# Kernel optimization log

Hardware: AMD Instinct MI355X
Metric: run time of the kernel (lower is better)

Reference implementation:

```python
import jax, jax.numpy as jnp
import numpy as np

AMP = 2  # from init_kwargs

def setup_inputs() -> dict:
    key = jax.random.key(0)
    k1, k2 = jax.random.split(key)
    B, C, H, W = 4, 32, 256, 256
    x_q = jax.random.normal(k1, (B, C, H, W), dtype=jnp.float32)
    x_k = jax.random.normal(k2, (B, C, H, W), dtype=jnp.float32)
    return {"x_q": x_q, "x_k": x_k, "num_heads": 4}


def reference(x_q, x_k, num_heads):
    amp = AMP
    ks = 2 * amp + 1  # kernel_size
    B, C, H, W = x_q.shape
    head_dim = C // num_heads
    scale = head_dim ** (-0.5)
    # (B, head_dim, heads, H, W)
    q = x_q.reshape(B, head_dim, num_heads, H, W) * scale
    k = x_k.reshape(B, head_dim, num_heads, H, W)
    k_pad = jnp.pad(k, ((0, 0), (0, 0), (0, 0), (amp, amp), (amp, amp)))
    # validity mask: padded region is invalid (mask < 0.5 in original)
    valid = jnp.pad(jnp.ones((H, W), dtype=x_q.dtype), ((amp, amp), (amp, amp)))
    attn = []
    for i in range(ks):  # static loop over 25 offsets
        for j in range(ks):
            # per-offset dot product over head_dim -> (B, heads, H, W)
            a = jnp.sum(q * k_pad[:, :, :, i:i + H, j:j + W], axis=1)
            a = jnp.where(valid[i:i + H, j:j + W] > 0.5, a, jnp.asarray(-1000.0, a.dtype))
            attn.append(a)
    attn = jnp.stack(attn, axis=1)          # (B, ks*ks, heads, H, W)
    attn = jax.nn.softmax(attn, axis=1)
    # offset grid: arange(-s//2+1, s//2+1) == [-amp, ..., amp]
    offs = jnp.arange(-amp, amp + 1, dtype=x_q.dtype)
    grid = jnp.stack(jnp.meshgrid(offs, offs, indexing='ij'), axis=-1).reshape(ks * ks, 2)
    # offset-weighted sum over the ks*ks window positions -> (B, 2, heads, H, W)
    v_ = jnp.einsum('bkhxy,kc->bchxy', attn, grid)
    # mean over heads -> (B, 2, H, W)
    return jnp.mean(v_, axis=2)
```

## Files before the change

### kernel.cpp

```cpp
#include <hip/hip_runtime.h>

#define Bdim 4
#define Cdim 32
#define NH   4
#define HD   8
#define Hdim 256
#define Wdim 256
#define AMP  2
#define KS   5

#define XT    32
#define TY    8
#define TROWS 12
#define TPOS  44
#define NPAIRS 16
#define PAIR_STRIDE (TROWS * TPOS)
#define TILE_SLOTS (NPAIRS * PAIR_STRIDE)

typedef _Float16 h2 __attribute__((ext_vector_type(2)));

static __device__ __forceinline__ float dot2acc(h2 a, h2 b, float c) {
#if __has_builtin(__builtin_amdgcn_fdot2)
    return __builtin_amdgcn_fdot2(a, b, c, false);
#else
    return c + (float)a.x * (float)b.x + (float)a.y * (float)b.y;
#endif
}

__global__ __launch_bounds__(256) void natt_offset_kernel(
    const float* __restrict__ xq,
    const float* __restrict__ xk,
    float* __restrict__ out)
{
    __shared__ __align__(16) float kt[TILE_SLOTS];

    const int tid = threadIdx.x;
    const int bid = blockIdx.x;
    const int r8  = bid & 7;
    const int u   = bid >> 3;
    const int yt  = r8 * 4 + (u & 3);
    const int rst = u >> 2;
    const int xt  = rst & 7;
    const int b   = rst >> 3;

    const int Y0 = yt * TY;
    const int X0 = xt * XT;
    const bool interior = (yt != 0) && (yt != 31) && (xt != 0) && (xt != 7);

    const int h    = tid >> 6;
    const int lane = tid & 63;
    const int row  = lane >> 3;
    const int qx   = lane & 7;
    const int y    = Y0 + row;
    const int x0   = X0 + qx * 4;

    const size_t plane = (size_t)Hdim * Wdim;
    const float scale = 0.35355339059327373f;

    {
        const float* kb = xk + (size_t)b * Cdim * plane;
        if (interior) {
            #pragma unroll
            for (int it = 0; it < 8; ++it) {
                const int j = lane + it * 64;
                if (j < NPAIRS / 4 * TROWS * 10) {
                    const int c4 = j % 10;
                    const int t  = j / 10;
                    const int rw = t % TROWS;
                    const int d2 = t / TROWS;
                    const int c0 = 8 * d2 + h;
                    const int yr = Y0 - AMP + rw;
                    const int xs = X0 - 6 + c4 * 4;
                    const float* pa = kb + (size_t)c0 * plane + (size_t)yr * Wdim + xs;
                    const float4 va = *(const float4*)pa;
                    const float4 vb = *(const float4*)(pa + 4 * plane);
                    const float a[4]  = {va.x, va.y, va.z, va.w};
                    const float bb[4] = {vb.x, vb.y, vb.z, vb.w};
                    float o[4];
                    #pragma unroll
                    for (int k2 = 0; k2 < 4; ++k2) {
                        h2 pk;
                        pk.x = (_Float16)a[k2];
                        pk.y = (_Float16)bb[k2];
                        o[k2] = __builtin_bit_cast(float, pk);
                    }
                    *(float4*)(kt + ((d2 << 2) | h) * PAIR_STRIDE + rw * TPOS + c4 * 4) =
                        make_float4(o[0], o[1], o[2], o[3]);
                }
            }
        } else {
            #pragma unroll
            for (int it = 0; it < 8; ++it) {
                const int j = lane + it * 64;
                if (j < NPAIRS / 4 * TROWS * 10) {
                    const int c4 = j % 10;
                    const int t  = j / 10;
                    const int rw = t % TROWS;
                    const int d2 = t / TROWS;
                    const int c0 = 8 * d2 + h;
                    int yr = Y0 - AMP + rw;
                    yr = yr < 0 ? 0 : (yr > Hdim - 1 ? Hdim - 1 : yr);
                    const int xs = X0 - 6 + c4 * 4;
                    const int xc = xs < 0 ? 0 : (xs > Wdim - 4 ? Wdim - 4 : xs);
                    const int sh = xs - xc;
                    const float* pa = kb + (size_t)c0 * plane + (size_t)yr * Wdim + xc;
                    const float4 va = *(const float4*)pa;
                    const float4 vb = *(const float4*)(pa + 4 * plane);
                    const float a[4]  = {va.x, va.y, va.z, va.w};
                    const float bb[4] = {vb.x, vb.y, vb.z, vb.w};
                    float o[4];
                    #pragma unroll
                    for (int k2 = 0; k2 < 4; ++k2) {
                        int idx = k2 + sh;
                        idx = idx < 0 ? 0 : (idx > 3 ? 3 : idx);
                        h2 pk;
                        pk.x = (_Float16)a[idx];
                        pk.y = (_Float16)bb[idx];
                        o[k2] = __builtin_bit_cast(float, pk);
                    }
                    *(float4*)(kt + ((d2 << 2) | h) * PAIR_STRIDE + rw * TPOS + c4 * 4) =
                        make_float4(o[0], o[1], o[2], o[3]);
                }
            }
        }
    }

    const float* qb = xq + (size_t)b * Cdim * plane + (size_t)y * Wdim + x0;
    h2 q2[4][4];
    #pragma unroll
    for (int d2 = 0; d2 < 4; ++d2) {
        const float4 qa = *(const float4*)(qb + (size_t)((2 * d2)     * NH + h) * plane);
        const float4 qc = *(const float4*)(qb + (size_t)((2 * d2 + 1) * NH + h) * plane);
        const float qa4[4] = {qa.x, qa.y, qa.z, qa.w};
        const float qc4[4] = {qc.x, qc.y, qc.z, qc.w};
        #pragma unroll
        for (int p = 0; p < 4; ++p) {
            q2[d2][p].x = (_Float16)(qa4[p] * scale);
            q2[d2][p].y = (_Float16)(qc4[p] * scale);
        }
    }


    float Z[4]  = {0.f, 0.f, 0.f, 0.f};
    float sx[4] = {0.f, 0.f, 0.f, 0.f};
    float sy[4] = {0.f, 0.f, 0.f, 0.f};

    #pragma unroll
    for (int r = 0; r < KS; ++r) {
        float dot[KS][4];
        #pragma unroll
        for (int dj = 0; dj < KS; ++dj) {
            dot[dj][0] = 0.f; dot[dj][1] = 0.f; dot[dj][2] = 0.f; dot[dj][3] = 0.f;
        }

        #pragma unroll
        for (int d2 = 0; d2 < 4; ++d2) {
            const float* wp = kt + ((d2 << 2) | h) * PAIR_STRIDE
                                 + (row + r) * TPOS + (qx * 4 + 4);
            const float4 wa = *(const float4*)wp;
            const float4 wb = *(const float4*)(wp + 4);
            const float wf[8] = {wa.x, wa.y, wa.z, wa.w, wb.x, wb.y, wb.z, wb.w};
            h2 w[8];
            #pragma unroll
            for (int k2 = 0; k2 < 8; ++k2) w[k2] = __builtin_bit_cast(h2, wf[k2]);
            #pragma unroll
            for (int dj = 0; dj < KS; ++dj) {
                #pragma unroll
                for (int p = 0; p < 4; ++p)
                    dot[dj][p] = dot2acc(q2[d2][p], w[p + dj], dot[dj][p]);
            }
        }

        const float fdi = (float)(r - AMP);
        if (interior) {
            #pragma unroll
            for (int p = 0; p < 4; ++p) {
                float e[KS];
                #pragma unroll
                for (int dj = 0; dj < KS; ++dj) e[dj] = __expf(dot[dj][p]);
                const float er = ((e[0] + e[1]) + (e[2] + e[3])) + e[4];
                Z[p]  += er;
                sx[p] += fdi * er;
                sy[p] += (e[3] - e[1]) + 2.f * (e[4] - e[0]);
            }
        } else {
            const int yy = y + r - AMP;
            const bool rowok = (yy >= 0) && (yy < Hdim);
            #pragma unroll
            for (int p = 0; p < 4; ++p) {
                float e[KS];
                #pragma unroll
                for (int dj = 0; dj < KS; ++dj) {
                    const int xx = x0 + p + dj - AMP;
                    const bool ok = rowok && (xx >= 0) && (xx < Wdim);
                    e[dj] = ok ? __expf(dot[dj][p]) : 0.f;
                }
                const float er = ((e[0] + e[1]) + (e[2] + e[3])) + e[4];
                Z[p]  += er;
                sx[p] += fdi * er;
                sy[p] += (e[3] - e[1]) + 2.f * (e[4] - e[0]);
            }
        }
    }

    __syncthreads();
    float* red = kt;
    const int pxl = row * XT + qx * 4;
    {
        const float i0 = 1.f / Z[0], i1 = 1.f / Z[1], i2 = 1.f / Z[2], i3 = 1.f / Z[3];
        *(float4*)(red + (h * 2 + 0) * (XT * TY) + pxl) =
            make_float4(sx[0]*i0, sx[1]*i1, sx[2]*i2, sx[3]*i3);
        *(float4*)(red + (h * 2 + 1) * (XT * TY) + pxl) =
            make_float4(sy[0]*i0, sy[1]*i1, sy[2]*i2, sy[3]*i3);
    }
    __syncthreads();

    if (h < 2) {
        float acc[4] = {0.f, 0.f, 0.f, 0.f};
        #pragma unroll
        for (int hh = 0; hh < NH; ++hh) {
            const float4 v = *(const float4*)(red + (hh * 2 + h) * (XT * TY) + pxl);
            acc[0] += v.x; acc[1] += v.y; acc[2] += v.z; acc[3] += v.w;
        }
        *(float4*)(out + ((size_t)b * 2 + h) * plane + (size_t)y * Wdim + x0) =
            make_float4(acc[0]*0.25f, acc[1]*0.25f, acc[2]*0.25f, acc[3]*0.25f);
    }
}

extern "C" void kernel_launch(void* const* d_in, const int* in_sizes, int n_in,
                              void* d_out, int out_size, void* d_ws, size_t ws_size,
                              hipStream_t stream) {
    const float* xq = (const float*)d_in[0];
    const float* xk = (const float*)d_in[1];
    float* out = (float*)d_out;

    natt_offset_kernel<<<dim3(1024, 1, 1), dim3(256, 1, 1), 0, stream>>>(xq, xk, out);
}
```

Before: 101.8 us.

## Split heads into separate 64-thread blocks and reduce heads with atomics

Each 256-thread block covering four heads becomes four 64-thread blocks, one per head, each holding a smaller shared K tile with tighter padding. The shared-memory cross-head reduction and its two barriers are replaced by float atomicAdds into an output that a new kernel zeroes first. The aim is more blocks, lower LDS per block and no block-level sync. In exchange it adds a second launch, four-way atomic contention per output element, and a summation order that is no longer deterministic.

```diff
diff --git a/kernel.cpp b/kernel.cpp
--- a/kernel.cpp
+++ b/kernel.cpp
@@ -12,8 +12,8 @@
 #define XT    32
 #define TY    8
 #define TROWS 12
-#define TPOS  44
-#define NPAIRS 16
+#define TPOS  40
+#define NPAIRS 4
 #define PAIR_STRIDE (TROWS * TPOS)
 #define TILE_SLOTS (NPAIRS * PAIR_STRIDE)
 
@@ -27,32 +27,36 @@
 #endif
 }
 
-__global__ __launch_bounds__(256) void natt_offset_kernel(
+__global__ __launch_bounds__(256) void zero_out_kernel(float* __restrict__ out) {
+    ((float4*)out)[blockIdx.x * 256 + threadIdx.x] = make_float4(0.f, 0.f, 0.f, 0.f);
+}
+
+__global__ __launch_bounds__(64, 4) void natt_head_kernel(
     const float* __restrict__ xq,
     const float* __restrict__ xk,
     float* __restrict__ out)
 {
     __shared__ __align__(16) float kt[TILE_SLOTS];
 
-    const int tid = threadIdx.x;
-    const int bid = blockIdx.x;
-    const int r8  = bid & 7;
+    const int lane = threadIdx.x;
+    const int bid  = blockIdx.x;
+    const int xcd = bid & 7;
     const int u   = bid >> 3;
-    const int yt  = r8 * 4 + (u & 3);
-    const int rst = u >> 2;
-    const int xt  = rst & 7;
-    const int b   = rst >> 3;
+    const int yt  = xcd * 4 + (u & 3);
+    const int v   = u >> 2;
+    const int xt  = v & 7;
+    const int w2  = v >> 3;
+    const int h   = w2 & 3;
+    const int b   = w2 >> 2;
 
     const int Y0 = yt * TY;
     const int X0 = xt * XT;
     const bool interior = (yt != 0) && (yt != 31) && (xt != 0) && (xt != 7);
 
-    const int h    = tid >> 6;
-    const int lane = tid & 63;
-    const int row  = lane >> 3;
-    const int qx   = lane & 7;
-    const int y    = Y0 + row;
-    const int x0   = X0 + qx * 4;
+    const int row = lane >> 3;
+    const int qx  = lane & 7;
+    const int y   = Y0 + row;
+    const int x0  = X0 + qx * 4;
 
     const size_t plane = (size_t)Hdim * Wdim;
     const float scale = 0.35355339059327373f;
@@ -63,7 +67,7 @@
             #pragma unroll
             for (int it = 0; it < 8; ++it) {
                 const int j = lane + it * 64;
-                if (j < NPAIRS / 4 * TROWS * 10) {
+                if (j < NPAIRS * TROWS * 10) {
                     const int c4 = j % 10;
                     const int t  = j / 10;
                     const int rw = t % TROWS;
@@ -84,7 +88,7 @@
                         pk.y = (_Float16)bb[k2];
                         o[k2] = __builtin_bit_cast(float, pk);
                     }
-                    *(float4*)(kt + ((d2 << 2) | h) * PAIR_STRIDE + rw * TPOS + c4 * 4) =
+                    *(float4*)(kt + d2 * PAIR_STRIDE + rw * TPOS + c4 * 4) =
                         make_float4(o[0], o[1], o[2], o[3]);
                 }
             }
@@ -92,7 +96,7 @@
             #pragma unroll
             for (int it = 0; it < 8; ++it) {
                 const int j = lane + it * 64;
-                if (j < NPAIRS / 4 * TROWS * 10) {
+                if (j < NPAIRS * TROWS * 10) {
                     const int c4 = j % 10;
                     const int t  = j / 10;
                     const int rw = t % TROWS;
@@ -118,7 +122,7 @@
                         pk.y = (_Float16)bb[idx];
                         o[k2] = __builtin_bit_cast(float, pk);
                     }
-                    *(float4*)(kt + ((d2 << 2) | h) * PAIR_STRIDE + rw * TPOS + c4 * 4) =
+                    *(float4*)(kt + d2 * PAIR_STRIDE + rw * TPOS + c4 * 4) =
                         make_float4(o[0], o[1], o[2], o[3]);
                 }
             }
@@ -155,8 +159,7 @@
 
         #pragma unroll
         for (int d2 = 0; d2 < 4; ++d2) {
-            const float* wp = kt + ((d2 << 2) | h) * PAIR_STRIDE
-                                 + (row + r) * TPOS + (qx * 4 + 4);
+            const float* wp = kt + d2 * PAIR_STRIDE + (row + r) * TPOS + (qx * 4 + 4);
             const float4 wa = *(const float4*)wp;
             const float4 wb = *(const float4*)(wp + 4);
             const float wf[8] = {wa.x, wa.y, wa.z, wa.w, wb.x, wb.y, wb.z, wb.w};
@@ -203,27 +206,12 @@
         }
     }
 
-    __syncthreads();
-    float* red = kt;
-    const int pxl = row * XT + qx * 4;
-    {
-        const float i0 = 1.f / Z[0], i1 = 1.f / Z[1], i2 = 1.f / Z[2], i3 = 1.f / Z[3];
-        *(float4*)(red + (h * 2 + 0) * (XT * TY) + pxl) =
-            make_float4(sx[0]*i0, sx[1]*i1, sx[2]*i2, sx[3]*i3);
-        *(float4*)(red + (h * 2 + 1) * (XT * TY) + pxl) =
-            make_float4(sy[0]*i0, sy[1]*i1, sy[2]*i2, sy[3]*i3);
-    }
-    __syncthreads();
-
-    if (h < 2) {
-        float acc[4] = {0.f, 0.f, 0.f, 0.f};
-        #pragma unroll
-        for (int hh = 0; hh < NH; ++hh) {
-            const float4 v = *(const float4*)(red + (hh * 2 + h) * (XT * TY) + pxl);
-            acc[0] += v.x; acc[1] += v.y; acc[2] += v.z; acc[3] += v.w;
-        }
-        *(float4*)(out + ((size_t)b * 2 + h) * plane + (size_t)y * Wdim + x0) =
-            make_float4(acc[0]*0.25f, acc[1]*0.25f, acc[2]*0.25f, acc[3]*0.25f);
+    float* o0 = out + (size_t)(b * 2) * plane + (size_t)y * Wdim + x0;
+    #pragma unroll
+    for (int p = 0; p < 4; ++p) {
+        const float inv = 0.25f / Z[p];
+        atomicAdd(o0 + p,         sx[p] * inv);
+        atomicAdd(o0 + plane + p, sy[p] * inv);
     }
 }
 
@@ -234,5 +222,6 @@
     const float* xk = (const float*)d_in[1];
     float* out = (float*)d_out;
 
-    natt_offset_kernel<<<dim3(1024, 1, 1), dim3(256, 1, 1), 0, stream>>>(xq, xk, out);
-}
+    zero_out_kernel<<<dim3(512, 1, 1), dim3(256, 1, 1), 0, stream>>>(out);
+    natt_head_kernel<<<dim3(4096, 1, 1), dim3(64, 1, 1), 0, stream>>>(xq, xk, out);
+}
```

Result: slower. 121.6 us (+19.5%).
